# Optimization experiments

Hardware: AMD Instinct MI355X
Metric: run time of the kernel (lower is better)

The kernel has to match this reference:

```python
import jax, jax.numpy as jnp
import numpy as np

L, K, V = 16, 2, 2
KV = K * V
S = 1 << L          # 65536 trellis states
R = 1 << (L - KV)   # 4096 reduced states
D = 1 << KV         # 16 candidate predecessors per state
B = 512             # viterbi batch rows


def _fp4_s1e2m1(x4):
    # x4: int array of 4-bit fp4 codes (s1e2m1, subnormal support)
    s = (x4 >> 3) & 1
    e = (x4 >> 1) & 3
    m = (x4 & 1).astype(np.float32)
    ef = e.astype(np.float32)
    val = np.where(e == 0, 0.5 * m, (1.0 + 0.5 * m) * np.exp2(ef - 1.0))
    return (val * np.where(s == 0, 1.0, -1.0)).astype(np.float32)


def _training_lut_fp4_v2():
    # CodebookLUTfreeFP4(L=16, V=2).get_training_lut()
    x = np.arange(S, dtype=np.int64)
    t = (((x + 1) * x) >> (16 - 8 - 1)) & 255   # big_index_to_small_index, 8-bit index
    pair = np.stack([(t >> 4) & 15, t & 15], axis=-1)  # int8_to_mx_pair -> [S, 2]
    lut = _fp4_s1e2m1(pair)
    return lut / lut.std(ddof=1)                 # torch .std() is unbiased


def setup_inputs() -> dict:
    key = jax.random.key(0)
    k1, k2 = jax.random.split(key)
    training_lut = jnp.asarray(_training_lut_fp4_v2(), dtype=jnp.float32)   # [S, V]
    cost = jax.random.uniform(k1, (B, S), dtype=jnp.float32) * 4.0          # running path costs
    orig_seq_part = jax.random.normal(k2, (B, V), dtype=jnp.float32)        # next V weights of each seq
    sumdelta = np.arange(D, dtype=np.int64) << (L - KV)                     # [D]
    base = (np.arange(S, dtype=np.int64) >> KV)[::D]                        # [R]
    state_candidates = jnp.asarray(base[:, None] + sumdelta[None, :], dtype=jnp.int32)  # [R, D]
    return {"training_lut": training_lut, "cost": cost,
            "orig_seq_part": orig_seq_part, "state_candidates": state_candidates}


def reference(training_lut, cost, orig_seq_part, state_candidates):
    # TrellisQuantizer.update: one Viterbi trellis transition
    Bb, Ss = cost.shape
    Rr, Dd = state_candidates.shape
    # gather candidate predecessor costs: cand_cost[b, r, d] = cost[b, state_candidates[r, d]]
    cand_cost = cost[:, state_candidates]                                   # [B, R, D]
    best_val = jnp.min(cand_cost, axis=-1)                                  # [B, R]
    best_idx = jnp.argmin(cand_cost, axis=-1)                               # [B, R]
    # squared error of every trellis state's codeword vs the observed V weights
    state_err = jnp.sum((training_lut[None, :, :] - orig_seq_part[:, None, :]) ** 2, axis=-1)  # [B, S]
    # expand best predecessor cost over the D states sharing it (view/expand/reshape in torch)
    new_cost = state_err + jnp.broadcast_to(best_val[:, :, None], (Bb, Rr, Dd)).reshape(Bb, Ss)
    # backpointer: which predecessor state won
    prev_state = state_candidates[jnp.arange(Rr)[None, :], best_idx]        # [B, R]
    return prev_state, new_cost
```

## Files before the change

kernel.cpp:

```cpp
#include <hip/hip_runtime.h>

constexpr int S_ = 1 << 16;
constexpr int R_ = 1 << 12;
constexpr int D_ = 16;
constexpr int B_ = 512;
constexpr int BLOCK = 256;
constexpr int RPT  = 4;
constexpr int RPB  = BLOCK * RPT;
constexpr int CHUNKS = R_ / RPB;

__global__ __launch_bounds__(256) void build_tab_kernel(
    const float* __restrict__ lut, float2* __restrict__ tab)
{
    const unsigned s = blockIdx.x * 256u + threadIdx.x;
    const unsigned t = (((s + 1u) * s) >> 7) & 255u;
    tab[t] = make_float2(lut[2 * s], lut[2 * s + 1]);
}

__global__ __launch_bounds__(BLOCK, 6) void trellis_kernel(
    const float*  __restrict__ cost,
    const float*  __restrict__ orig,
    const float2* __restrict__ tab,
    float*        __restrict__ prev_state_out,
    float*        __restrict__ new_cost)
{
    __shared__ float lds_bv[RPB];
    __shared__ float lds_err[256];

    const int b      = blockIdx.x / CHUNKS;
    const int rchunk = blockIdx.x % CHUNKS;
    const int r0     = rchunk * RPB;
    const int tid    = threadIdx.x;

    const float  o0 = orig[2 * b + 0];
    const float  o1 = orig[2 * b + 1];
    const float2 tv = tab[tid];

    const int r = r0 + tid * RPT;
    const float* pb = cost + (size_t)b * S_ + r;

    float4 bv = *(const float4*)pb;
    int bia = 0, bib = 0, bic = 0, bid_ = 0;
    #pragma unroll
    for (int d = 1; d < D_; ++d) {
        const float4 v = *(const float4*)(pb + (size_t)d * R_);
        if (v.x < bv.x) { bv.x = v.x; bia  = d; }
        if (v.y < bv.y) { bv.y = v.y; bib  = d; }
        if (v.z < bv.z) { bv.z = v.z; bic  = d; }
        if (v.w < bv.w) { bv.w = v.w; bid_ = d; }
    }

    *(float4*)(prev_state_out + (size_t)b * R_ + r) =
        make_float4((float)(r     + (bia  << 12)),
                    (float)(r + 1 + (bib  << 12)),
                    (float)(r + 2 + (bic  << 12)),
                    (float)(r + 3 + (bid_ << 12)));

    *(float4*)(lds_bv + tid * RPT) = bv;

    {
        const float e0 = tv.x - o0, e1 = tv.y - o1;
        lds_err[tid] = e0 * e0 + e1 * e1;
    }
    __syncthreads();

    const int s_base = r0 << 4;
    float* outb = new_cost + (size_t)b * S_ + s_base;
    #pragma unroll
    for (int it = 0; it < (RPB * D_) / (BLOCK * 4); ++it) {
        const int flat = it * (BLOCK * 4) + tid * 4;
        const unsigned s = (unsigned)(s_base + flat);
        const float bvv = lds_bv[flat >> 4];
        float4 out;
        out.x = lds_err[(((s + 1u) * (s + 0u)) >> 7) & 255u] + bvv;
        out.y = lds_err[(((s + 2u) * (s + 1u)) >> 7) & 255u] + bvv;
        out.z = lds_err[(((s + 3u) * (s + 2u)) >> 7) & 255u] + bvv;
        out.w = lds_err[(((s + 4u) * (s + 3u)) >> 7) & 255u] + bvv;
        *(float4*)(outb + flat) = out;
    }
}

extern "C" void kernel_launch(void* const* d_in, const int* in_sizes, int n_in,
                              void* d_out, int out_size, void* d_ws, size_t ws_size,
                              hipStream_t stream) {
    const float* lut  = (const float*)d_in[0];
    const float* cost = (const float*)d_in[1];
    const float* orig = (const float*)d_in[2];

    float* prev_state = (float*)d_out;
    float* new_cost   = (float*)d_out + (size_t)B_ * R_;
    float2* tab       = (float2*)d_ws;

    hipLaunchKernelGGL(build_tab_kernel, dim3(S_ / 256), dim3(256), 0, stream,
                       lut, tab);
    hipLaunchKernelGGL(trellis_kernel, dim3(B_ * CHUNKS), dim3(BLOCK), 0, stream,
                       cost, orig, tab, prev_state, new_cost);
}
```

Measured before the change: 255.4 us.

## Process two row chunks per block, overlapping next chunk loads with stores

Each block now handles two 1024-state chunks of a batch row instead of one. It issues all 16 candidate loads for the second chunk through inline-asm global_load_dwordx4 before writing the first chunk's results, so reads overlap the output stores. The expanded store loop is remapped per wave, so each wave reads only the best values it wrote itself and needs no block barrier. The cost is higher register pressure: launch bounds drop to 4 waves per SIMD, and the hand-written asm with explicit vmcnt waits is more brittle.

After: 256.4 us. Within noise of the previous version (+0.4%).

```diff
diff --git a/kernel.cpp b/kernel.cpp
--- a/kernel.cpp
+++ b/kernel.cpp
@@ -7,7 +7,9 @@
 constexpr int BLOCK = 256;
 constexpr int RPT  = 4;
 constexpr int RPB  = BLOCK * RPT;
-constexpr int CHUNKS = R_ / RPB;
+constexpr int PAIRS = R_ / (2 * RPB);
+
+typedef float v4f __attribute__((ext_vector_type(4)));
 
 __global__ __launch_bounds__(256) void build_tab_kernel(
     const float* __restrict__ lut, float2* __restrict__ tab)
@@ -17,7 +19,77 @@
     tab[t] = make_float2(lut[2 * s], lut[2 * s + 1]);
 }
 
-__global__ __launch_bounds__(BLOCK, 6) void trellis_kernel(
+#define ISSUE16(P, SB, OFF) asm volatile(                      \
+    "global_load_dwordx4 %[c0], %[off], %[sb]\n\t"             \
+    "v_add_u32 %[off], 0x4000, %[off]\n\t"                     \
+    "global_load_dwordx4 %[c1], %[off], %[sb]\n\t"             \
+    "v_add_u32 %[off], 0x4000, %[off]\n\t"                     \
+    "global_load_dwordx4 %[c2], %[off], %[sb]\n\t"             \
+    "v_add_u32 %[off], 0x4000, %[off]\n\t"                     \
+    "global_load_dwordx4 %[c3], %[off], %[sb]\n\t"             \
+    "v_add_u32 %[off], 0x4000, %[off]\n\t"                     \
+    "global_load_dwordx4 %[c4], %[off], %[sb]\n\t"             \
+    "v_add_u32 %[off], 0x4000, %[off]\n\t"                     \
+    "global_load_dwordx4 %[c5], %[off], %[sb]\n\t"             \
+    "v_add_u32 %[off], 0x4000, %[off]\n\t"                     \
+    "global_load_dwordx4 %[c6], %[off], %[sb]\n\t"             \
+    "v_add_u32 %[off], 0x4000, %[off]\n\t"                     \
+    "global_load_dwordx4 %[c7], %[off], %[sb]\n\t"             \
+    "v_add_u32 %[off], 0x4000, %[off]\n\t"                     \
+    "global_load_dwordx4 %[c8], %[off], %[sb]\n\t"             \
+    "v_add_u32 %[off], 0x4000, %[off]\n\t"                     \
+    "global_load_dwordx4 %[c9], %[off], %[sb]\n\t"             \
+    "v_add_u32 %[off], 0x4000, %[off]\n\t"                     \
+    "global_load_dwordx4 %[c10], %[off], %[sb]\n\t"            \
+    "v_add_u32 %[off], 0x4000, %[off]\n\t"                     \
+    "global_load_dwordx4 %[c11], %[off], %[sb]\n\t"            \
+    "v_add_u32 %[off], 0x4000, %[off]\n\t"                     \
+    "global_load_dwordx4 %[c12], %[off], %[sb]\n\t"            \
+    "v_add_u32 %[off], 0x4000, %[off]\n\t"                     \
+    "global_load_dwordx4 %[c13], %[off], %[sb]\n\t"            \
+    "v_add_u32 %[off], 0x4000, %[off]\n\t"                     \
+    "global_load_dwordx4 %[c14], %[off], %[sb]\n\t"            \
+    "v_add_u32 %[off], 0x4000, %[off]\n\t"                     \
+    "global_load_dwordx4 %[c15], %[off], %[sb]"                \
+    : [c0]"=&v"(P##0),  [c1]"=&v"(P##1),  [c2]"=&v"(P##2),     \
+      [c3]"=&v"(P##3),  [c4]"=&v"(P##4),  [c5]"=&v"(P##5),     \
+      [c6]"=&v"(P##6),  [c7]"=&v"(P##7),  [c8]"=&v"(P##8),     \
+      [c9]"=&v"(P##9),  [c10]"=&v"(P##10), [c11]"=&v"(P##11),  \
+      [c12]"=&v"(P##12), [c13]"=&v"(P##13), [c14]"=&v"(P##14), \
+      [c15]"=&v"(P##15), [off]"+v"(OFF)                        \
+    : [sb]"s"(SB) : "memory")
+
+#define VMWAIT() do { asm volatile("s_waitcnt vmcnt(0)" ::: "memory"); \
+                      __builtin_amdgcn_sched_barrier(0); } while (0)
+
+#define AMIN(dd, cc)                                   \
+    if (cc[0] < bva) { bva = cc[0]; bia  = dd; }       \
+    if (cc[1] < bvb) { bvb = cc[1]; bib  = dd; }       \
+    if (cc[2] < bvc) { bvc = cc[2]; bic  = dd; }       \
+    if (cc[3] < bvd) { bvd = cc[3]; bid_ = dd; }
+
+__device__ __forceinline__ void store_chunk(
+    float* __restrict__ rowo, const float* lds_bv, const float* lds_err,
+    int rbase, int wave, int lane)
+{
+    const int sw_f = (rbase + wave * 256) << 4;
+    float* outw = rowo + sw_f;
+    const int bvbase = wave * 256;
+    #pragma unroll
+    for (int it = 0; it < 16; ++it) {
+        const int fl = it * 256 + lane * 4;
+        const unsigned s = (unsigned)(sw_f + fl);
+        const float bvv = lds_bv[bvbase + it * 16 + (lane >> 2)];
+        float4 out;
+        out.x = lds_err[(((s + 1u) * (s + 0u)) >> 7) & 255u] + bvv;
+        out.y = lds_err[(((s + 2u) * (s + 1u)) >> 7) & 255u] + bvv;
+        out.z = lds_err[(((s + 3u) * (s + 2u)) >> 7) & 255u] + bvv;
+        out.w = lds_err[(((s + 4u) * (s + 3u)) >> 7) & 255u] + bvv;
+        *(float4*)(outw + fl) = out;
+    }
+}
+
+__global__ __launch_bounds__(BLOCK, 4) void trellis_kernel(
     const float*  __restrict__ cost,
     const float*  __restrict__ orig,
     const float2* __restrict__ tab,
@@ -27,57 +99,74 @@
     __shared__ float lds_bv[RPB];
     __shared__ float lds_err[256];
 
-    const int b      = blockIdx.x / CHUNKS;
-    const int rchunk = blockIdx.x % CHUNKS;
-    const int r0     = rchunk * RPB;
-    const int tid    = threadIdx.x;
+    const int b    = blockIdx.x / PAIRS;
+    const int pair = blockIdx.x % PAIRS;
+    const int r0   = pair * (2 * RPB);
+    const int r1   = r0 + RPB;
+    const int tid  = threadIdx.x;
+    const int wave = tid >> 6;
+    const int lane = tid & 63;
 
     const float  o0 = orig[2 * b + 0];
     const float  o1 = orig[2 * b + 1];
     const float2 tv = tab[tid];
-
-    const int r = r0 + tid * RPT;
-    const float* pb = cost + (size_t)b * S_ + r;
-
-    float4 bv = *(const float4*)pb;
-    int bia = 0, bib = 0, bic = 0, bid_ = 0;
-    #pragma unroll
-    for (int d = 1; d < D_; ++d) {
-        const float4 v = *(const float4*)(pb + (size_t)d * R_);
-        if (v.x < bv.x) { bv.x = v.x; bia  = d; }
-        if (v.y < bv.y) { bv.y = v.y; bib  = d; }
-        if (v.z < bv.z) { bv.z = v.z; bic  = d; }
-        if (v.w < bv.w) { bv.w = v.w; bid_ = d; }
-    }
-
-    *(float4*)(prev_state_out + (size_t)b * R_ + r) =
-        make_float4((float)(r     + (bia  << 12)),
-                    (float)(r + 1 + (bib  << 12)),
-                    (float)(r + 2 + (bic  << 12)),
-                    (float)(r + 3 + (bid_ << 12)));
-
-    *(float4*)(lds_bv + tid * RPT) = bv;
-
     {
         const float e0 = tv.x - o0, e1 = tv.y - o1;
         lds_err[tid] = e0 * e0 + e1 * e1;
     }
     __syncthreads();
 
-    const int s_base = r0 << 4;
-    float* outb = new_cost + (size_t)b * S_ + s_base;
-    #pragma unroll
-    for (int it = 0; it < (RPB * D_) / (BLOCK * 4); ++it) {
-        const int flat = it * (BLOCK * 4) + tid * 4;
-        const unsigned s = (unsigned)(s_base + flat);
-        const float bvv = lds_bv[flat >> 4];
-        float4 out;
-        out.x = lds_err[(((s + 1u) * (s + 0u)) >> 7) & 255u] + bvv;
-        out.y = lds_err[(((s + 2u) * (s + 1u)) >> 7) & 255u] + bvv;
-        out.z = lds_err[(((s + 3u) * (s + 2u)) >> 7) & 255u] + bvv;
-        out.w = lds_err[(((s + 4u) * (s + 3u)) >> 7) & 255u] + bvv;
-        *(float4*)(outb + flat) = out;
+    const float* rowc = cost + (size_t)b * S_;
+    float* rowo    = new_cost       + (size_t)b * S_;
+    float* prevrow = prev_state_out + (size_t)b * R_;
+
+    v4f c0, c1, c2, c3, c4, c5, c6, c7, c8, c9, c10, c11, c12, c13, c14, c15;
+    unsigned off0 = (unsigned)tid * 16u;
+    const float* sb0 = rowc + r0;
+    ISSUE16(c, sb0, off0);
+    VMWAIT();
+
+    float bva = c0[0], bvb = c0[1], bvc = c0[2], bvd = c0[3];
+    int bia = 0, bib = 0, bic = 0, bid_ = 0;
+    AMIN(1, c1)  AMIN(2, c2)  AMIN(3, c3)  AMIN(4, c4)
+    AMIN(5, c5)  AMIN(6, c6)  AMIN(7, c7)  AMIN(8, c8)
+    AMIN(9, c9)  AMIN(10, c10) AMIN(11, c11) AMIN(12, c12)
+    AMIN(13, c13) AMIN(14, c14) AMIN(15, c15)
+
+    v4f e0, e1, e2, e3, e4, e5, e6, e7, e8, e9, e10, e11, e12, e13, e14, e15;
+    unsigned off1 = (unsigned)tid * 16u;
+    const float* sb1 = rowc + r1;
+    ISSUE16(e, sb1, off1);
+
+    {
+        const int r = r0 + tid * RPT;
+        *(float4*)(prevrow + r) =
+            make_float4((float)(r     + (bia  << 12)),
+                        (float)(r + 1 + (bib  << 12)),
+                        (float)(r + 2 + (bic  << 12)),
+                        (float)(r + 3 + (bid_ << 12)));
+        *(float4*)(lds_bv + tid * RPT) = make_float4(bva, bvb, bvc, bvd);
     }
+    store_chunk(rowo, lds_bv, lds_err, r0, wave, lane);
+
+    VMWAIT();
+    bva = e0[0]; bvb = e0[1]; bvc = e0[2]; bvd = e0[3];
+    bia = 0; bib = 0; bic = 0; bid_ = 0;
+    AMIN(1, e1)  AMIN(2, e2)  AMIN(3, e3)  AMIN(4, e4)
+    AMIN(5, e5)  AMIN(6, e6)  AMIN(7, e7)  AMIN(8, e8)
+    AMIN(9, e9)  AMIN(10, e10) AMIN(11, e11) AMIN(12, e12)
+    AMIN(13, e13) AMIN(14, e14) AMIN(15, e15)
+
+    {
+        const int r = r1 + tid * RPT;
+        *(float4*)(prevrow + r) =
+            make_float4((float)(r     + (bia  << 12)),
+                        (float)(r + 1 + (bib  << 12)),
+                        (float)(r + 2 + (bic  << 12)),
+                        (float)(r + 3 + (bid_ << 12)));
+        *(float4*)(lds_bv + tid * RPT) = make_float4(bva, bvb, bvc, bvd);
+    }
+    store_chunk(rowo, lds_bv, lds_err, r1, wave, lane);
 }
 
 extern "C" void kernel_launch(void* const* d_in, const int* in_sizes, int n_in,
@@ -93,6 +182,6 @@
 
     hipLaunchKernelGGL(build_tab_kernel, dim3(S_ / 256), dim3(256), 0, stream,
                        lut, tab);
-    hipLaunchKernelGGL(trellis_kernel, dim3(B_ * CHUNKS), dim3(BLOCK), 0, stream,
+    hipLaunchKernelGGL(trellis_kernel, dim3(B_ * PAIRS), dim3(BLOCK), 0, stream,
                        cost, orig, tab, prev_state, new_cost);
 }
```
